# Kernel tuning notes

Hardware: AMD Instinct MI355X
Metric: run time of the kernel (lower is better)

## Reference

```python
import jax, jax.numpy as jnp
import numpy as np

B, S, D = 4, 4096, 1024
P = int(D * 1.333)  # 1364, matches torch int(d_model * proj_factor)
CAP = 15.0
EPS = 1e-6


def _rmsnorm(x, w, eps=EPS):
    xf = x.astype(jnp.float32)
    var = jnp.mean(xf * xf, axis=-1, keepdims=True)
    return w * (xf * jax.lax.rsqrt(var + eps)).astype(x.dtype)


def _softcap_sigmoid(g):
    # sigmoid(cap * tanh(g / cap))
    return jax.nn.sigmoid(CAP * jnp.tanh(g / CAP))


def setup_inputs() -> dict:
    key = jax.random.key(0)
    k0, k1, k2, k3 = jax.random.split(key, 4)
    x = jax.random.normal(k0, (B, S, D), jnp.float32)
    hidden_state = jnp.zeros((B, P), jnp.float32)
    ln_weight = jnp.ones((D,), jnp.float32)
    W_gate = jax.random.normal(k1, (D, 3 * P), jnp.float32) / np.sqrt(D).astype(np.float32)
    W_cell = jax.random.normal(k2, (D, P), jnp.float32) / np.sqrt(D).astype(np.float32)
    W_out = jax.random.normal(k3, (P, D), jnp.float32) / np.sqrt(P).astype(np.float32)
    return {"x": x, "hidden_state": hidden_state, "ln_weight": ln_weight,
            "W_gate": W_gate, "W_cell": W_cell, "W_out": W_out}


def reference(x, hidden_state, ln_weight, W_gate, W_cell, W_out):
    b, s, d = x.shape
    residual = x
    xn = _rmsnorm(x, ln_weight)
    # gate projection -> [b, s, 3, P], unbind gate types
    gates = jnp.einsum('bsd,dk->bsk', xn, W_gate).reshape(b, s, 3, P)
    i_gate = _softcap_sigmoid(gates[:, :, 0])
    f_gate = _softcap_sigmoid(gates[:, :, 1])
    o_gate = _softcap_sigmoid(gates[:, :, 2])
    c_input = jnp.einsum('bsd,dp->bsp', xn, W_cell)

    # sequential linear recurrence: h_t = f_t * h_{t-1} + i_t * tanh(c_t)
    def step(h, inp):
        c_t, i_t, f_t, o_t = inp
        h = f_t * h + i_t * jnp.tanh(c_t)
        return h, o_t * jnp.tanh(h)

    seq = (jnp.swapaxes(c_input, 0, 1), jnp.swapaxes(i_gate, 0, 1),
           jnp.swapaxes(f_gate, 0, 1), jnp.swapaxes(o_gate, 0, 1))  # time-major [s,b,P]
    _, outs = jax.lax.scan(step, hidden_state, seq)
    outputs = jnp.swapaxes(outs, 0, 1)  # [b, s, P]

    out = residual + jnp.einsum('bsp,pd->bsd', outputs, W_out)
    # NOTE: original torch module returns the UNMODIFIED initial hidden_state
    return out, hidden_state
```

## Files before the change

### kernel.cpp

```cpp
#include <hip/hip_runtime.h>
#include <hip/hip_bf16.h>
#include <math.h>
#include <stdint.h>

typedef __bf16 bf16_t;
typedef bf16_t bf16x4 __attribute__((ext_vector_type(4)));
typedef bf16_t bf16x8 __attribute__((ext_vector_type(8)));
typedef float floatx4 __attribute__((ext_vector_type(4)));

#define B_     4
#define S_     4096
#define D_     1024
#define P_     1364
#define P3_    4092
#define NP_    5456
#define NPAD_  5504
#define NB_    5632
#define KPAD_  1408
#define ROWS_  16384
#define CAP_   15.0f
#define EPS_   1e-6f
#define CHUNKS_ 32
#define CLEN_   128

__device__ __forceinline__ float fast_tanh(float x) {
    x = fminf(fmaxf(x, -15.f), 15.f);
    float e = __expf(2.f * x);
    return __fdividef(e - 1.f, e + 1.f);
}
__device__ __forceinline__ float fast_softcap_sig(float g) {
    float t = fast_tanh(g * (1.0f / CAP_));
    return __fdividef(1.f, 1.f + __expf(-CAP_ * t));
}

template <int N>
__device__ __forceinline__ void vmcnt_wait() {
    if constexpr (N == 8)      asm volatile("s_waitcnt vmcnt(8)" ::: "memory");
    else if constexpr (N == 4) asm volatile("s_waitcnt vmcnt(4)" ::: "memory");
    else if constexpr (N == 0) asm volatile("s_waitcnt vmcnt(0)" ::: "memory");
}

__global__ __launch_bounds__(256) void rmsnorm_kernel(const float* __restrict__ x,
                                                      const float* __restrict__ w,
                                                      bf16_t* __restrict__ xn) {
    int row = blockIdx.x;
    int tid = threadIdx.x;
    const float4 v = ((const float4*)(x + (size_t)row * D_))[tid];
    float ss = v.x * v.x + v.y * v.y + v.z * v.z + v.w * v.w;
    #pragma unroll
    for (int off = 32; off > 0; off >>= 1) ss += __shfl_down(ss, off);
    __shared__ float red[4];
    if ((tid & 63) == 0) red[tid >> 6] = ss;
    __syncthreads();
    float tot = red[0] + red[1] + red[2] + red[3];
    float scale = rsqrtf(tot * (1.0f / (float)D_) + EPS_);
    const float4 wv = ((const float4*)w)[tid];
    bf16x4 o;
    o[0] = (bf16_t)(v.x * scale * wv.x);
    o[1] = (bf16_t)(v.y * scale * wv.y);
    o[2] = (bf16_t)(v.z * scale * wv.z);
    o[3] = (bf16_t)(v.w * scale * wv.w);
    ((bf16x4*)(xn + (size_t)row * D_))[tid] = o;
}

__global__ __launch_bounds__(256) void pack_wcat(const float* __restrict__ Wg,
                                                 const float* __restrict__ Wc,
                                                 bf16_t* __restrict__ Wt) {
    __shared__ float tile[32][33];
    int kt = blockIdx.x * 32;
    int nt = blockIdx.y * 32;
    int tx = threadIdx.x & 31;
    int ty = threadIdx.x >> 5;
    #pragma unroll
    for (int i = 0; i < 4; i++) {
        int k = kt + ty + 8 * i;
        int n = nt + tx;
        float val = 0.f;
        if (n < P3_)      val = Wg[(size_t)k * P3_ + n];
        else if (n < NP_) val = Wc[(size_t)k * P_ + (n - P3_)];
        tile[ty + 8 * i][tx] = val;
    }
    __syncthreads();
    #pragma unroll
    for (int i = 0; i < 4; i++) {
        int n = nt + ty + 8 * i;
        int k = kt + tx;
        Wt[(size_t)n * D_ + k] = (bf16_t)tile[tx][ty + 8 * i];
    }
}

__global__ __launch_bounds__(256) void pack_wout(const float* __restrict__ Wo,
                                                 bf16_t* __restrict__ Wt) {
    __shared__ float tile[32][33];
    int pt = blockIdx.x * 32;
    int dt = blockIdx.y * 32;
    int tx = threadIdx.x & 31;
    int ty = threadIdx.x >> 5;
    #pragma unroll
    for (int i = 0; i < 4; i++) {
        int p = pt + ty + 8 * i;
        int d = dt + tx;
        float val = (p < P_) ? Wo[(size_t)p * D_ + d] : 0.f;
        tile[ty + 8 * i][tx] = val;
    }
    __syncthreads();
    #pragma unroll
    for (int i = 0; i < 4; i++) {
        int d = dt + ty + 8 * i;
        int p = pt + tx;
        Wt[(size_t)d * KPAD_ + p] = (bf16_t)tile[tx][ty + 8 * i];
    }
}


#define PH_SYNC                                                               \
    __builtin_amdgcn_s_barrier();                                             \
    asm volatile("s_waitcnt lgkmcnt(0)" ::: "memory");                        \
    __builtin_amdgcn_sched_barrier(0);

#define MFMA_ROW(NLO)                                                         \
    _Pragma("unroll")                                                         \
    for (int m = 0; m < 8; m++) {                                             \
      acc[m][NLO]     = __builtin_amdgcn_mfma_f32_16x16x32_bf16(af[m], b0, acc[m][NLO], 0, 0, 0);     \
      acc[m][NLO + 1] = __builtin_amdgcn_mfma_f32_16x16x32_bf16(af[m], b1, acc[m][NLO + 1], 0, 0, 0); \
    }

#define K_ITER(KT, CB, DO_NXT, DO_CUR, VMA, VMB)                              \
  {                                                                           \
    _Pragma("unroll") for (int m = 0; m < 8; m++) af[m] = ldA(CB, 0, m);      \
    b0 = ldB(CB, 0, 0); b1 = ldB(CB, 0, 1);                                   \
    if (DO_NXT) stA((KT) + 1, 1, (CB) ^ 1);                                   \
    PH_SYNC                                                                   \
    __builtin_amdgcn_s_setprio(1);                                            \
    MFMA_ROW(0)                                                               \
    __builtin_amdgcn_s_setprio(0);                                            \
    __builtin_amdgcn_s_barrier();                                             \
    b0 = ldB(CB, 0, 2); b1 = ldB(CB, 0, 3);                                   \
    if (DO_NXT) stB((KT) + 1, 1, (CB) ^ 1);                                   \
    PH_SYNC                                                                   \
    __builtin_amdgcn_s_setprio(1);                                            \
    MFMA_ROW(2)                                                               \
    __builtin_amdgcn_s_setprio(0);                                            \
    vmcnt_wait<VMA>();                                                        \
    __builtin_amdgcn_s_barrier();                                             \
    _Pragma("unroll") for (int m = 0; m < 8; m++) af[m] = ldA(CB, 1, m);      \
    b0 = ldB(CB, 1, 0); b1 = ldB(CB, 1, 1);                                   \
    if (DO_CUR) stA((KT) + 2, 0, (CB));                                       \
    PH_SYNC                                                                   \
    __builtin_amdgcn_s_setprio(1);                                            \
    MFMA_ROW(0)                                                               \
    __builtin_amdgcn_s_setprio(0);                                            \
    __builtin_amdgcn_s_barrier();                                             \
    b0 = ldB(CB, 1, 2); b1 = ldB(CB, 1, 3);                                   \
    if (DO_CUR) stB((KT) + 2, 0, (CB));                                       \
    PH_SYNC                                                                   \
    __builtin_amdgcn_s_setprio(1);                                            \
    MFMA_ROW(2)                                                               \
    __builtin_amdgcn_s_setprio(0);                                            \
    vmcnt_wait<VMB>();                                                        \
    __builtin_amdgcn_s_barrier();                                             \
  }

template <int KTOT, int LDA, int LDB, int LDC, int NX, int EPI>
__global__ __launch_bounds__(512, 2) void gemm8(const bf16_t* __restrict__ A,
                                                const bf16_t* __restrict__ Bt,
                                                const float* __restrict__ res,
                                                void* __restrict__ outv) {
    constexpr int NT = KTOT / 64;
    static_assert(NT % 2 == 0 && NT >= 4, "NT must be even, >=4");
    __shared__ __align__(16) char smem[131072];

    const int tid  = threadIdx.x;
    const int wid  = tid >> 6;
    const int lane = tid & 63;
    const int l15  = lane & 15;
    const int sl4  = lane >> 4;
    const int sp    = sl4 ^ ((lane >> 1) & 3);
    const int chunk = (lane & 3) ^ ((lane >> 3) & 3);
    const int wrow = (wid >> 2) * 128;
    const int wcol = (wid & 3) * 64;

    constexpr int NWG = NX * (ROWS_ / 256);
    constexpr int CPX = NWG / 8;
    int lin = blockIdx.x;
    lin = (lin & 7) * CPX + (lin >> 3);
    const int by = lin / NX, bx = lin % NX;
    const int m0 = by * 256, n0 = bx * 256;

    const int srow = wid * 16 + (lane >> 2);
    const bf16_t* Asrc = A  + (size_t)(m0 + srow) * LDA + chunk * 8;
    const bf16_t* Bsrc = Bt + (size_t)(n0 + srow) * LDB + chunk * 8;
    const unsigned ldsA0 = (unsigned)(wid * 1024);
    const unsigned ldsB0 = 32768u + (unsigned)(wid * 1024);

    auto stA = [&](int kt, int kk, int buf) {
        const bf16_t* s = Asrc + kt * 64 + kk * 32;
        char* d = smem + ((unsigned)buf * 65536u + (unsigned)kk * 16384u + ldsA0);
        __builtin_amdgcn_global_load_lds((const unsigned*)s, (unsigned*)d, 16, 0, 0);
        __builtin_amdgcn_global_load_lds((const unsigned*)(s + (size_t)128 * LDA),
                                         (unsigned*)(d + 8192), 16, 0, 0);
    };
    auto stB = [&](int kt, int kk, int buf) {
        const bf16_t* s = Bsrc + kt * 64 + kk * 32;
        char* d = smem + ((unsigned)buf * 65536u + (unsigned)kk * 16384u + ldsB0);
        __builtin_amdgcn_global_load_lds((const unsigned*)s, (unsigned*)d, 16, 0, 0);
        __builtin_amdgcn_global_load_lds((const unsigned*)(s + (size_t)128 * LDB),
                                         (unsigned*)(d + 8192), 16, 0, 0);
    };
    auto ldA = [&](int buf, int kk, int m) -> bf16x8 {
        return *(const bf16x8*)(smem + (buf * 65536 + kk * 16384 +
                                        (wrow + m * 16 + l15) * 64 + sp * 16));
    };
    auto ldB = [&](int buf, int kk, int n) -> bf16x8 {
        return *(const bf16x8*)(smem + (buf * 65536 + 32768 + kk * 16384 +
                                        (wcol + n * 16 + l15) * 64 + sp * 16));
    };

    floatx4 acc[8][4];
    #pragma unroll
    for (int m = 0; m < 8; m++)
        #pragma unroll
        for (int n = 0; n < 4; n++) acc[m][n] = (floatx4){0.f, 0.f, 0.f, 0.f};
    bf16x8 af[8], b0, b1;

    stA(0, 0, 0); stB(0, 0, 0);
    stA(0, 1, 0); stB(0, 1, 0);
    stA(1, 0, 1); stB(1, 0, 1);
    vmcnt_wait<8>();
    __builtin_amdgcn_s_barrier();

    for (int kt = 0; kt < NT - 2; kt += 2) {
        K_ITER(kt,     0, true, true, 8, 8)
        K_ITER(kt + 1, 1, true, true, 8, 8)
    }
    K_ITER(NT - 2, 0, true,  false, 8, 4)
    K_ITER(NT - 1, 1, false, false, 0, -1)

    const int crow = m0 + wrow + sl4 * 4;
    const int ccol = n0 + wcol + l15;
    if constexpr (EPI == 0) {
        bf16_t* O = (bf16_t*)outv;
        #pragma unroll
        for (int m = 0; m < 8; m++)
            #pragma unroll
            for (int n = 0; n < 4; n++) {
                const int col = ccol + n * 16;
                if (col < NPAD_) {
                    #pragma unroll
                    for (int r = 0; r < 4; r++) {
                        const int row = crow + m * 16 + r;
                        float g = acc[m][n][r];
                        float v = (col < P3_) ? fast_softcap_sig(g) : fast_tanh(g);
                        O[(size_t)row * LDC + col] = (bf16_t)v;
                    }
                }
            }
    } else {
        float* O = (float*)outv;
        #pragma unroll
        for (int m = 0; m < 8; m++)
            #pragma unroll
            for (int n = 0; n < 4; n++) {
                const int col = ccol + n * 16;
                #pragma unroll
                for (int r = 0; r < 4; r++) {
                    const int row = crow + m * 16 + r;
                    O[(size_t)row * LDC + col] = res[(size_t)row * LDC + col] + acc[m][n][r];
                }
            }
    }
}

__global__ __launch_bounds__(256) void chunk_scan1(const bf16_t* __restrict__ act,
                                                   float* __restrict__ FA) {
    int p = blockIdx.x * 256 + threadIdx.x;
    int c = blockIdx.y;
    int b = blockIdx.z;
    if (p >= P_) return;
    const bf16_t* base = act + (size_t)(b * S_ + c * CLEN_) * NPAD_;
    float F = 1.f, Acc = 0.f;
    for (int t = 0; t < CLEN_; t++) {
        const bf16_t* r = base + (size_t)t * NPAD_;
        float iv = (float)r[p];
        float fv = (float)r[P_ + p];
        float tc = (float)r[P3_ + p];
        Acc = fv * Acc + iv * tc;
        F *= fv;
    }
    size_t idx = (((size_t)b * CHUNKS_ + c) * P_ + p) * 2;
    FA[idx]     = F;
    FA[idx + 1] = Acc;
}

__global__ __launch_bounds__(256) void chunk_scan2(const bf16_t* __restrict__ act,
                                                   const float* __restrict__ FA,
                                                   const float* __restrict__ h0,
                                                   bf16_t* __restrict__ outp) {
    int p = blockIdx.x * 256 + threadIdx.x;
    int c = blockIdx.y;
    int b = blockIdx.z;
    if (p >= KPAD_) return;
    if (p >= P_) {
        bf16_t z = (bf16_t)0.f;
        for (int t = 0; t < CLEN_; t++)
            outp[(size_t)(b * S_ + c * CLEN_ + t) * KPAD_ + p] = z;
        return;
    }
    float h = h0[(size_t)b * P_ + p];
    for (int j = 0; j < c; j++) {
        size_t idx = (((size_t)b * CHUNKS_ + j) * P_ + p) * 2;
        h = FA[idx + 1] + FA[idx] * h;
    }
    const bf16_t* base = act + (size_t)(b * S_ + c * CLEN_) * NPAD_;
    bf16_t* ob = outp + (size_t)(b * S_ + c * CLEN_) * KPAD_;
    for (int t = 0; t < CLEN_; t++) {
        const bf16_t* r = base + (size_t)t * NPAD_;
        float iv = (float)r[p];
        float fv = (float)r[P_ + p];
        float ov = (float)r[2 * P_ + p];
        float tc = (float)r[P3_ + p];
        h = fv * h + iv * tc;
        ob[(size_t)t * KPAD_ + p] = (bf16_t)(ov * fast_tanh(h));
    }
}

__global__ void copy_hidden(const float* __restrict__ hs, float* __restrict__ dst) {
    int i = blockIdx.x * 256 + threadIdx.x;
    if (i < B_ * P_) dst[i] = hs[i];
}

extern "C" void kernel_launch(void* const* d_in, const int* in_sizes, int n_in,
                              void* d_out, int out_size, void* d_ws, size_t ws_size,
                              hipStream_t stream) {
    const float* x   = (const float*)d_in[0];
    const float* hs  = (const float*)d_in[1];
    const float* lnw = (const float*)d_in[2];
    const float* Wg  = (const float*)d_in[3];
    const float* Wc  = (const float*)d_in[4];
    const float* Wo  = (const float*)d_in[5];
    float* out = (float*)d_out;

    char* ws = (char*)d_ws;
    size_t off = 0;
    auto alloc = [&](size_t bytes) {
        void* p = ws + off;
        off += (bytes + 255) & ~(size_t)255;
        return p;
    };
    bf16_t* xn_outp = (bf16_t*)alloc((size_t)ROWS_ * KPAD_ * 2);
    bf16_t* act     = (bf16_t*)alloc((size_t)ROWS_ * NPAD_ * 2);
    bf16_t* WcatT   = (bf16_t*)alloc((size_t)NB_ * D_ * 2);
    bf16_t* WoutT   = (bf16_t*)alloc((size_t)D_ * KPAD_ * 2);
    float*  FA      = (float*)alloc((size_t)B_ * CHUNKS_ * P_ * 2 * 4);

    bf16_t* xn   = xn_outp;
    bf16_t* outp = xn_outp;

    hipLaunchKernelGGL(rmsnorm_kernel, dim3(ROWS_), dim3(256), 0, stream, x, lnw, xn);
    hipLaunchKernelGGL(pack_wcat, dim3(32, NB_ / 32), dim3(256), 0, stream, Wg, Wc, WcatT);
    hipLaunchKernelGGL(pack_wout, dim3(KPAD_ / 32, D_ / 32), dim3(256), 0, stream, Wo, WoutT);

    hipLaunchKernelGGL((gemm8<D_, D_, D_, NPAD_, NB_ / 256, 0>),
                       dim3((NB_ / 256) * (ROWS_ / 256)), dim3(512), 0, stream,
                       xn, WcatT, (const float*)nullptr, (void*)act);

    hipLaunchKernelGGL(chunk_scan1, dim3(6, CHUNKS_, B_), dim3(256), 0, stream, act, FA);
    hipLaunchKernelGGL(chunk_scan2, dim3(6, CHUNKS_, B_), dim3(256), 0, stream, act, FA, hs, outp);

    hipLaunchKernelGGL((gemm8<KPAD_, KPAD_, KPAD_, D_, D_ / 256, 1>),
                       dim3((D_ / 256) * (ROWS_ / 256)), dim3(512), 0, stream,
                       outp, WoutT, x, d_out);

    hipLaunchKernelGGL(copy_hidden, dim3((B_ * P_ + 255) / 256), dim3(256), 0, stream,
                       hs, out + (size_t)ROWS_ * D_);
}
```

Baseline: 467.0 us.

## Simplify GEMM pipeline, remap tiles, pad gate layout, vectorize chunked scan

Replaces the hand-interleaved half-tile MFMA/LDS schedule with a simpler double-buffered loop that stages a full K tile and computes it between two barriers. Block-to-tile mapping now keeps each XCD on a contiguous band of M rows. The activation buffer is re-laid out with each gate padded to 1368 columns so the scan kernels can do 16-byte bf16x8 loads and stores. Chunk count rises to 64 with 64-step chunks, and each scan thread handles 8 channels. Risks include a less overlapped GEMM schedule, fewer scan blocks per chunk, and a longer serial prefix combine in the second scan.

After: 639.3 us. 36.9% more time.

```diff
diff --git a/kernel.cpp b/kernel.cpp
--- a/kernel.cpp
+++ b/kernel.cpp
@@ -14,14 +14,15 @@
 #define P_     1364
 #define P3_    4092
 #define NP_    5456
-#define NPAD_  5504
 #define NB_    5632
+#define PR_    1368
+#define ACT_LD_ 5472
 #define KPAD_  1408
 #define ROWS_  16384
 #define CAP_   15.0f
 #define EPS_   1e-6f
-#define CHUNKS_ 32
-#define CLEN_   128
+#define CHUNKS_ 64
+#define CLEN_   64
 
 __device__ __forceinline__ float fast_tanh(float x) {
     x = fminf(fmaxf(x, -15.f), 15.f);
@@ -36,7 +37,6 @@
 template <int N>
 __device__ __forceinline__ void vmcnt_wait() {
     if constexpr (N == 8)      asm volatile("s_waitcnt vmcnt(8)" ::: "memory");
-    else if constexpr (N == 4) asm volatile("s_waitcnt vmcnt(4)" ::: "memory");
     else if constexpr (N == 0) asm volatile("s_waitcnt vmcnt(0)" ::: "memory");
 }
 
@@ -112,62 +112,13 @@
     }
 }
 
-
-#define PH_SYNC                                                               \
-    __builtin_amdgcn_s_barrier();                                             \
-    asm volatile("s_waitcnt lgkmcnt(0)" ::: "memory");                        \
-    __builtin_amdgcn_sched_barrier(0);
-
-#define MFMA_ROW(NLO)                                                         \
-    _Pragma("unroll")                                                         \
-    for (int m = 0; m < 8; m++) {                                             \
-      acc[m][NLO]     = __builtin_amdgcn_mfma_f32_16x16x32_bf16(af[m], b0, acc[m][NLO], 0, 0, 0);     \
-      acc[m][NLO + 1] = __builtin_amdgcn_mfma_f32_16x16x32_bf16(af[m], b1, acc[m][NLO + 1], 0, 0, 0); \
-    }
-
-#define K_ITER(KT, CB, DO_NXT, DO_CUR, VMA, VMB)                              \
-  {                                                                           \
-    _Pragma("unroll") for (int m = 0; m < 8; m++) af[m] = ldA(CB, 0, m);      \
-    b0 = ldB(CB, 0, 0); b1 = ldB(CB, 0, 1);                                   \
-    if (DO_NXT) stA((KT) + 1, 1, (CB) ^ 1);                                   \
-    PH_SYNC                                                                   \
-    __builtin_amdgcn_s_setprio(1);                                            \
-    MFMA_ROW(0)                                                               \
-    __builtin_amdgcn_s_setprio(0);                                            \
-    __builtin_amdgcn_s_barrier();                                             \
-    b0 = ldB(CB, 0, 2); b1 = ldB(CB, 0, 3);                                   \
-    if (DO_NXT) stB((KT) + 1, 1, (CB) ^ 1);                                   \
-    PH_SYNC                                                                   \
-    __builtin_amdgcn_s_setprio(1);                                            \
-    MFMA_ROW(2)                                                               \
-    __builtin_amdgcn_s_setprio(0);                                            \
-    vmcnt_wait<VMA>();                                                        \
-    __builtin_amdgcn_s_barrier();                                             \
-    _Pragma("unroll") for (int m = 0; m < 8; m++) af[m] = ldA(CB, 1, m);      \
-    b0 = ldB(CB, 1, 0); b1 = ldB(CB, 1, 1);                                   \
-    if (DO_CUR) stA((KT) + 2, 0, (CB));                                       \
-    PH_SYNC                                                                   \
-    __builtin_amdgcn_s_setprio(1);                                            \
-    MFMA_ROW(0)                                                               \
-    __builtin_amdgcn_s_setprio(0);                                            \
-    __builtin_amdgcn_s_barrier();                                             \
-    b0 = ldB(CB, 1, 2); b1 = ldB(CB, 1, 3);                                   \
-    if (DO_CUR) stB((KT) + 2, 0, (CB));                                       \
-    PH_SYNC                                                                   \
-    __builtin_amdgcn_s_setprio(1);                                            \
-    MFMA_ROW(2)                                                               \
-    __builtin_amdgcn_s_setprio(0);                                            \
-    vmcnt_wait<VMB>();                                                        \
-    __builtin_amdgcn_s_barrier();                                             \
-  }
-
 template <int KTOT, int LDA, int LDB, int LDC, int NX, int EPI>
 __global__ __launch_bounds__(512, 2) void gemm8(const bf16_t* __restrict__ A,
                                                 const bf16_t* __restrict__ Bt,
                                                 const float* __restrict__ res,
                                                 void* __restrict__ outv) {
     constexpr int NT = KTOT / 64;
-    static_assert(NT % 2 == 0 && NT >= 4, "NT must be even, >=4");
+    static_assert(NT >= 4, "NT >= 4");
     __shared__ __align__(16) char smem[131072];
 
     const int tid  = threadIdx.x;
@@ -180,11 +131,13 @@
     const int wrow = (wid >> 2) * 128;
     const int wcol = (wid & 3) * 64;
 
-    constexpr int NWG = NX * (ROWS_ / 256);
-    constexpr int CPX = NWG / 8;
-    int lin = blockIdx.x;
-    lin = (lin & 7) * CPX + (lin >> 3);
-    const int by = lin / NX, bx = lin % NX;
+    constexpr int MB  = ROWS_ / 256;
+    constexpr int MCH = MB / 8;
+    const int bid = blockIdx.x;
+    const int xcd = bid & 7;
+    const int idx = bid >> 3;
+    const int bx  = idx / MCH;
+    const int by  = xcd * MCH + (idx - bx * MCH);
     const int m0 = by * 256, n0 = bx * 256;
 
     const int srow = wid * 16 + (lane >> 2);
@@ -193,19 +146,20 @@
     const unsigned ldsA0 = (unsigned)(wid * 1024);
     const unsigned ldsB0 = 32768u + (unsigned)(wid * 1024);
 
-    auto stA = [&](int kt, int kk, int buf) {
-        const bf16_t* s = Asrc + kt * 64 + kk * 32;
-        char* d = smem + ((unsigned)buf * 65536u + (unsigned)kk * 16384u + ldsA0);
-        __builtin_amdgcn_global_load_lds((const unsigned*)s, (unsigned*)d, 16, 0, 0);
-        __builtin_amdgcn_global_load_lds((const unsigned*)(s + (size_t)128 * LDA),
-                                         (unsigned*)(d + 8192), 16, 0, 0);
-    };
-    auto stB = [&](int kt, int kk, int buf) {
-        const bf16_t* s = Bsrc + kt * 64 + kk * 32;
-        char* d = smem + ((unsigned)buf * 65536u + (unsigned)kk * 16384u + ldsB0);
-        __builtin_amdgcn_global_load_lds((const unsigned*)s, (unsigned*)d, 16, 0, 0);
-        __builtin_amdgcn_global_load_lds((const unsigned*)(s + (size_t)128 * LDB),
-                                         (unsigned*)(d + 8192), 16, 0, 0);
+    auto stage = [&](int kt, int buf) {
+        #pragma unroll
+        for (int kk = 0; kk < 2; kk++) {
+            const bf16_t* sa = Asrc + kt * 64 + kk * 32;
+            char* da = smem + ((unsigned)buf * 65536u + (unsigned)kk * 16384u + ldsA0);
+            __builtin_amdgcn_global_load_lds((const unsigned*)sa, (unsigned*)da, 16, 0, 0);
+            __builtin_amdgcn_global_load_lds((const unsigned*)(sa + (size_t)128 * LDA),
+                                             (unsigned*)(da + 8192), 16, 0, 0);
+            const bf16_t* sb = Bsrc + kt * 64 + kk * 32;
+            char* db = smem + ((unsigned)buf * 65536u + (unsigned)kk * 16384u + ldsB0);
+            __builtin_amdgcn_global_load_lds((const unsigned*)sb, (unsigned*)db, 16, 0, 0);
+            __builtin_amdgcn_global_load_lds((const unsigned*)(sb + (size_t)128 * LDB),
+                                             (unsigned*)(db + 8192), 16, 0, 0);
+        }
     };
     auto ldA = [&](int buf, int kk, int m) -> bf16x8 {
         return *(const bf16x8*)(smem + (buf * 65536 + kk * 16384 +
@@ -221,20 +175,46 @@
     for (int m = 0; m < 8; m++)
         #pragma unroll
         for (int n = 0; n < 4; n++) acc[m][n] = (floatx4){0.f, 0.f, 0.f, 0.f};
-    bf16x8 af[8], b0, b1;
-
-    stA(0, 0, 0); stB(0, 0, 0);
-    stA(0, 1, 0); stB(0, 1, 0);
-    stA(1, 0, 1); stB(1, 0, 1);
+
+    auto compute_tile = [&](int buf) {
+        bf16x8 a[8], bb[4];
+        #pragma unroll
+        for (int kk = 0; kk < 2; kk++) {
+            #pragma unroll
+            for (int m = 0; m < 8; m++) a[m] = ldA(buf, kk, m);
+            #pragma unroll
+            for (int n = 0; n < 4; n++) bb[n] = ldB(buf, kk, n);
+            #pragma unroll
+            for (int m = 0; m < 8; m++)
+                #pragma unroll
+                for (int n = 0; n < 4; n++)
+                    acc[m][n] = __builtin_amdgcn_mfma_f32_16x16x32_bf16(a[m], bb[n], acc[m][n], 0, 0, 0);
+        }
+    };
+
+    stage(0, 0);
+    stage(1, 1);
     vmcnt_wait<8>();
     __builtin_amdgcn_s_barrier();
 
-    for (int kt = 0; kt < NT - 2; kt += 2) {
-        K_ITER(kt,     0, true, true, 8, 8)
-        K_ITER(kt + 1, 1, true, true, 8, 8)
-    }
-    K_ITER(NT - 2, 0, true,  false, 8, 4)
-    K_ITER(NT - 1, 1, false, false, 0, -1)
+    #pragma unroll 2
+    for (int t = 0; t < NT - 1; ++t) {
+        const int cur = t & 1;
+        __builtin_amdgcn_s_setprio(1);
+        compute_tile(cur);
+        __builtin_amdgcn_s_setprio(0);
+        __builtin_amdgcn_s_barrier();
+        if (t + 2 < NT) {
+            stage(t + 2, cur);
+            vmcnt_wait<8>();
+        } else {
+            vmcnt_wait<0>();
+        }
+        __builtin_amdgcn_s_barrier();
+    }
+    __builtin_amdgcn_s_setprio(1);
+    compute_tile((NT - 1) & 1);
+    __builtin_amdgcn_s_setprio(0);
 
     const int crow = m0 + wrow + sl4 * 4;
     const int ccol = n0 + wcol + l15;
@@ -245,13 +225,16 @@
             #pragma unroll
             for (int n = 0; n < 4; n++) {
                 const int col = ccol + n * 16;
-                if (col < NPAD_) {
+                if (col < NP_) {
+                    const int g  = (col >= P3_) ? 3 : col / P_;
+                    const int pp = col - g * P_;
+                    const size_t cb = (size_t)g * PR_ + pp;
                     #pragma unroll
                     for (int r = 0; r < 4; r++) {
                         const int row = crow + m * 16 + r;
-                        float g = acc[m][n][r];
-                        float v = (col < P3_) ? fast_softcap_sig(g) : fast_tanh(g);
-                        O[(size_t)row * LDC + col] = (bf16_t)v;
+                        float gg = acc[m][n][r];
+                        float v = (g < 3) ? fast_softcap_sig(gg) : fast_tanh(gg);
+                        O[(size_t)row * LDC + cb] = (bf16_t)v;
                     }
                 }
             }
@@ -273,54 +256,112 @@
 
 __global__ __launch_bounds__(256) void chunk_scan1(const bf16_t* __restrict__ act,
                                                    float* __restrict__ FA) {
-    int p = blockIdx.x * 256 + threadIdx.x;
-    int c = blockIdx.y;
-    int b = blockIdx.z;
-    if (p >= P_) return;
-    const bf16_t* base = act + (size_t)(b * S_ + c * CLEN_) * NPAD_;
-    float F = 1.f, Acc = 0.f;
-    for (int t = 0; t < CLEN_; t++) {
-        const bf16_t* r = base + (size_t)t * NPAD_;
-        float iv = (float)r[p];
-        float fv = (float)r[P_ + p];
-        float tc = (float)r[P3_ + p];
-        Acc = fv * Acc + iv * tc;
-        F *= fv;
-    }
-    size_t idx = (((size_t)b * CHUNKS_ + c) * P_ + p) * 2;
-    FA[idx]     = F;
-    FA[idx + 1] = Acc;
+    int p8 = (blockIdx.x * 256 + threadIdx.x) * 8;
+    if (p8 >= P_) return;
+    int c = blockIdx.y, b = blockIdx.z;
+    const bf16_t* base = act + (size_t)(b * S_ + c * CLEN_) * ACT_LD_;
+    float F[8], Ac[8];
+    #pragma unroll
+    for (int e = 0; e < 8; e++) { F[e] = 1.f; Ac[e] = 0.f; }
+    if (p8 + 8 <= P_) {
+        for (int t = 0; t < CLEN_; t++) {
+            const bf16_t* r = base + (size_t)t * ACT_LD_;
+            bf16x8 iv = *(const bf16x8*)(r + p8);
+            bf16x8 fv = *(const bf16x8*)(r + PR_ + p8);
+            bf16x8 tc = *(const bf16x8*)(r + 3 * PR_ + p8);
+            #pragma unroll
+            for (int e = 0; e < 8; e++) {
+                float f = (float)fv[e];
+                Ac[e] = f * Ac[e] + (float)iv[e] * (float)tc[e];
+                F[e] *= f;
+            }
+        }
+    } else {
+        for (int t = 0; t < CLEN_; t++) {
+            const bf16_t* r = base + (size_t)t * ACT_LD_;
+            #pragma unroll
+            for (int e = 0; e < 8; e++) {
+                int p = p8 + e;
+                if (p < P_) {
+                    float f = (float)r[PR_ + p];
+                    Ac[e] = f * Ac[e] + (float)r[p] * (float)r[3 * PR_ + p];
+                    F[e] *= f;
+                }
+            }
+        }
+    }
+    #pragma unroll
+    for (int e = 0; e < 8; e++) {
+        int p = p8 + e;
+        if (p < P_) {
+            size_t idx = (((size_t)b * CHUNKS_ + c) * P_ + p) * 2;
+            FA[idx] = F[e]; FA[idx + 1] = Ac[e];
+        }
+    }
 }
 
 __global__ __launch_bounds__(256) void chunk_scan2(const bf16_t* __restrict__ act,
                                                    const float* __restrict__ FA,
                                                    const float* __restrict__ h0,
                                                    bf16_t* __restrict__ outp) {
-    int p = blockIdx.x * 256 + threadIdx.x;
-    int c = blockIdx.y;
-    int b = blockIdx.z;
-    if (p >= KPAD_) return;
-    if (p >= P_) {
-        bf16_t z = (bf16_t)0.f;
+    int p8 = (blockIdx.x * 256 + threadIdx.x) * 8;
+    if (p8 >= KPAD_) return;
+    int c = blockIdx.y, b = blockIdx.z;
+    bf16_t* ob = outp + (size_t)(b * S_ + c * CLEN_) * KPAD_;
+    if (p8 >= P_) {
+        bf16x8 z;
+        #pragma unroll
+        for (int e = 0; e < 8; e++) z[e] = (bf16_t)0.f;
         for (int t = 0; t < CLEN_; t++)
-            outp[(size_t)(b * S_ + c * CLEN_ + t) * KPAD_ + p] = z;
+            *(bf16x8*)(ob + (size_t)t * KPAD_ + p8) = z;
         return;
     }
-    float h = h0[(size_t)b * P_ + p];
+    float h[8];
+    #pragma unroll
+    for (int e = 0; e < 8; e++) {
+        int p = p8 + e;
+        h[e] = (p < P_) ? h0[(size_t)b * P_ + p] : 0.f;
+    }
     for (int j = 0; j < c; j++) {
-        size_t idx = (((size_t)b * CHUNKS_ + j) * P_ + p) * 2;
-        h = FA[idx + 1] + FA[idx] * h;
-    }
-    const bf16_t* base = act + (size_t)(b * S_ + c * CLEN_) * NPAD_;
-    bf16_t* ob = outp + (size_t)(b * S_ + c * CLEN_) * KPAD_;
-    for (int t = 0; t < CLEN_; t++) {
-        const bf16_t* r = base + (size_t)t * NPAD_;
-        float iv = (float)r[p];
-        float fv = (float)r[P_ + p];
-        float ov = (float)r[2 * P_ + p];
-        float tc = (float)r[P3_ + p];
-        h = fv * h + iv * tc;
-        ob[(size_t)t * KPAD_ + p] = (bf16_t)(ov * fast_tanh(h));
+        #pragma unroll
+        for (int e = 0; e < 8; e++) {
+            int p = p8 + e;
+            if (p < P_) {
+                size_t idx = (((size_t)b * CHUNKS_ + j) * P_ + p) * 2;
+                h[e] = FA[idx + 1] + FA[idx] * h[e];
+            }
+        }
+    }
+    const bf16_t* base = act + (size_t)(b * S_ + c * CLEN_) * ACT_LD_;
+    if (p8 + 8 <= P_) {
+        for (int t = 0; t < CLEN_; t++) {
+            const bf16_t* r = base + (size_t)t * ACT_LD_;
+            bf16x8 iv = *(const bf16x8*)(r + p8);
+            bf16x8 fv = *(const bf16x8*)(r + PR_ + p8);
+            bf16x8 ov = *(const bf16x8*)(r + 2 * PR_ + p8);
+            bf16x8 tc = *(const bf16x8*)(r + 3 * PR_ + p8);
+            bf16x8 o;
+            #pragma unroll
+            for (int e = 0; e < 8; e++) {
+                h[e] = (float)fv[e] * h[e] + (float)iv[e] * (float)tc[e];
+                o[e] = (bf16_t)((float)ov[e] * fast_tanh(h[e]));
+            }
+            *(bf16x8*)(ob + (size_t)t * KPAD_ + p8) = o;
+        }
+    } else {
+        for (int t = 0; t < CLEN_; t++) {
+            const bf16_t* r = base + (size_t)t * ACT_LD_;
+            #pragma unroll
+            for (int e = 0; e < 8; e++) {
+                int p = p8 + e;
+                bf16_t val = (bf16_t)0.f;
+                if (p < P_) {
+                    h[e] = (float)r[PR_ + p] * h[e] + (float)r[p] * (float)r[3 * PR_ + p];
+                    val = (bf16_t)((float)r[2 * PR_ + p] * fast_tanh(h[e]));
+                }
+                ob[(size_t)t * KPAD_ + p] = val;
+            }
+        }
     }
 }
 
@@ -348,7 +389,7 @@
         return p;
     };
     bf16_t* xn_outp = (bf16_t*)alloc((size_t)ROWS_ * KPAD_ * 2);
-    bf16_t* act     = (bf16_t*)alloc((size_t)ROWS_ * NPAD_ * 2);
+    bf16_t* act     = (bf16_t*)alloc((size_t)ROWS_ * ACT_LD_ * 2);
     bf16_t* WcatT   = (bf16_t*)alloc((size_t)NB_ * D_ * 2);
     bf16_t* WoutT   = (bf16_t*)alloc((size_t)D_ * KPAD_ * 2);
     float*  FA      = (float*)alloc((size_t)B_ * CHUNKS_ * P_ * 2 * 4);
@@ -360,12 +401,12 @@
     hipLaunchKernelGGL(pack_wcat, dim3(32, NB_ / 32), dim3(256), 0, stream, Wg, Wc, WcatT);
     hipLaunchKernelGGL(pack_wout, dim3(KPAD_ / 32, D_ / 32), dim3(256), 0, stream, Wo, WoutT);
 
-    hipLaunchKernelGGL((gemm8<D_, D_, D_, NPAD_, NB_ / 256, 0>),
+    hipLaunchKernelGGL((gemm8<D_, D_, D_, ACT_LD_, NB_ / 256, 0>),
                        dim3((NB_ / 256) * (ROWS_ / 256)), dim3(512), 0, stream,
                        xn, WcatT, (const float*)nullptr, (void*)act);
 
-    hipLaunchKernelGGL(chunk_scan1, dim3(6, CHUNKS_, B_), dim3(256), 0, stream, act, FA);
-    hipLaunchKernelGGL(chunk_scan2, dim3(6, CHUNKS_, B_), dim3(256), 0, stream, act, FA, hs, outp);
+    hipLaunchKernelGGL(chunk_scan1, dim3(1, CHUNKS_, B_), dim3(256), 0, stream, act, FA);
+    hipLaunchKernelGGL(chunk_scan2, dim3(1, CHUNKS_, B_), dim3(256), 0, stream, act, FA, hs, outp);
 
     hipLaunchKernelGGL((gemm8<KPAD_, KPAD_, KPAD_, D_, D_ / 256, 1>),
                        dim3((D_ / 256) * (ROWS_ / 256)), dim3(512), 0, stream,
```
